# Performance work log

Hardware: AMD Instinct MI355X
Metric: run time of the kernel (lower is better)

## Reference

```python
import jax, jax.numpy as jnp
import numpy as np

B, S, D = 4, 2048, 1024
H, DK = 16, 64  # num_head, d_k = d_model // num_head
THETA = 10000.0


def apply_rope(x, positions):
    # x: [B, H, S, DK], positions: [S] int
    half = DK // 2
    inv_freq = THETA ** (-jnp.arange(half, dtype=jnp.float32) * 2.0 / DK)  # [half]
    angles = positions.astype(jnp.float32)[:, None] * inv_freq[None, :]    # [S, half]
    cos, sin = jnp.cos(angles), jnp.sin(angles)                            # [S, half]
    x1 = x[..., 0::2]  # [B,H,S,half]
    x2 = x[..., 1::2]
    r1 = x1 * cos - x2 * sin
    r2 = x1 * sin + x2 * cos
    # re-interleave pairs back to [B,H,S,DK]
    return jnp.stack([r1, r2], axis=-1).reshape(x.shape)


def setup_inputs() -> dict:
    key = jax.random.key(0)
    kx, kq, kk, kv, ko = jax.random.split(key, 5)
    scale = 1.0 / np.sqrt(D)
    return {
        "x": jax.random.normal(kx, (B, S, D), dtype=jnp.float32),
        "Wq": jax.random.normal(kq, (D, D), dtype=jnp.float32) * scale,
        "Wk": jax.random.normal(kk, (D, D), dtype=jnp.float32) * scale,
        "Wv": jax.random.normal(kv, (D, D), dtype=jnp.float32) * scale,
        "Wo": jax.random.normal(ko, (D, D), dtype=jnp.float32) * scale,
        "token_positions": jnp.arange(S, dtype=jnp.int64 if jax.config.jax_enable_x64 else jnp.int32),
    }


def reference(x, Wq, Wk, Wv, Wo, token_positions):
    # Projections (torch Linear convention: y = x @ W.T, no bias)
    def proj(x, W):
        return (x @ W.T).reshape(B, S, H, DK).transpose(0, 2, 1, 3)  # [B,H,S,DK]

    Q = apply_rope(proj(x, Wq), token_positions)
    K = apply_rope(proj(x, Wk), token_positions)
    V = proj(x, Wv)

    scores = jnp.einsum('bhqd,bhkd->bhqk', Q, K) / np.sqrt(DK)  # [B,H,S,S]
    causal = jnp.tril(jnp.ones((S, S), dtype=bool))
    scores = jnp.where(causal, scores, -jnp.inf)
    attn = jax.nn.softmax(scores, axis=-1)
    out = jnp.einsum('bhqk,bhkd->bhqd', attn, V)               # [B,H,S,DK]
    out = out.transpose(0, 2, 1, 3).reshape(B, S, D)
    return out @ Wo.T
```

## Files before the change

kernel.cpp:

```cpp
#include <hip/hip_runtime.h>
#include <math.h>

#define S_LEN  2048
#define D_DIM  1024
#define NHEAD  16
#define HDK    64
#define NBATCH 4

typedef __attribute__((ext_vector_type(8))) short bf16x8;
typedef __attribute__((ext_vector_type(4))) float f32x4;

#define MFMA16(a, b, c) __builtin_amdgcn_mfma_f32_16x16x32_bf16((a), (b), (c), 0, 0, 0)


__device__ __forceinline__ unsigned short f2bf(float f) {
    unsigned u = __float_as_uint(f);
    u += 0x7fffu + ((u >> 16) & 1u);
    return (unsigned short)(u >> 16);
}

__device__ __forceinline__ void barrier_keep_vmem() {
    asm volatile("s_waitcnt lgkmcnt(0)" ::: "memory");
    __builtin_amdgcn_s_barrier();
    __builtin_amdgcn_sched_barrier(0);
}

__global__ __launch_bounds__(256)
void convert_kernel(const float* __restrict__ src, unsigned short* __restrict__ dst, int n)
{
    int i = (blockIdx.x * 256 + threadIdx.x) * 8;
    if (i >= n) return;
    float4 f0 = *(const float4*)&src[i];
    float4 f1 = *(const float4*)&src[i + 4];
    uint4 o;
    o.x = f2bf(f0.x) | ((unsigned)f2bf(f0.y) << 16);
    o.y = f2bf(f0.z) | ((unsigned)f2bf(f0.w) << 16);
    o.z = f2bf(f1.x) | ((unsigned)f2bf(f1.y) << 16);
    o.w = f2bf(f1.z) | ((unsigned)f2bf(f1.w) << 16);
    *(uint4*)&dst[i] = o;
}

__global__ __launch_bounds__(256)
void proj_qkv_kernel(const unsigned short* __restrict__ Xb,
                     const unsigned short* __restrict__ Wqb,
                     const unsigned short* __restrict__ Wkb,
                     const unsigned short* __restrict__ Wvb,
                     const int* __restrict__ pos,
                     unsigned short* __restrict__ Qb,
                     unsigned short* __restrict__ Kb,
                     unsigned short* __restrict__ Vtb)
{
    __shared__ short As[128][40];
    __shared__ short Bs[128][40];

    const int t  = threadIdx.x;
    const int l  = t & 63;
    const int w  = t >> 6;
    const int wr = w >> 1, wc = w & 1;
    const int lm = l & 15;
    const int lk = (l >> 4) * 8;

    const int nb   = blockIdx.x;
    const int wsel = nb >> 3;
    const int n0   = (nb & 7) * 128;
    const int m0   = blockIdx.y * 128;
    const unsigned short* W = (wsel == 0) ? Wqb : (wsel == 1) ? Wkb : Wvb;

    const int sr = t >> 2;
    const int sc = (t & 3) * 8;

    f32x4 acc[4][4];
#pragma unroll
    for (int i = 0; i < 4; ++i)
#pragma unroll
        for (int j = 0; j < 4; ++j) acc[i][j] = (f32x4){0.f, 0.f, 0.f, 0.f};

    uint4 a0 = *(const uint4*)&Xb[(size_t)(m0 + sr)      * D_DIM + sc];
    uint4 a1 = *(const uint4*)&Xb[(size_t)(m0 + sr + 64) * D_DIM + sc];
    uint4 b0 = *(const uint4*)&W [(size_t)(n0 + sr)      * D_DIM + sc];
    uint4 b1 = *(const uint4*)&W [(size_t)(n0 + sr + 64) * D_DIM + sc];

    for (int k0 = 0; k0 < D_DIM; k0 += 32) {
        __syncthreads();
        *(uint4*)&As[sr][sc]      = a0;
        *(uint4*)&As[sr + 64][sc] = a1;
        *(uint4*)&Bs[sr][sc]      = b0;
        *(uint4*)&Bs[sr + 64][sc] = b1;
        if (k0 + 32 < D_DIM) {
            a0 = *(const uint4*)&Xb[(size_t)(m0 + sr)      * D_DIM + k0 + 32 + sc];
            a1 = *(const uint4*)&Xb[(size_t)(m0 + sr + 64) * D_DIM + k0 + 32 + sc];
            b0 = *(const uint4*)&W [(size_t)(n0 + sr)      * D_DIM + k0 + 32 + sc];
            b1 = *(const uint4*)&W [(size_t)(n0 + sr + 64) * D_DIM + k0 + 32 + sc];
        }
        barrier_keep_vmem();

        bf16x8 af[4], bf[4];
#pragma unroll
        for (int mt = 0; mt < 4; ++mt)
            af[mt] = *(const bf16x8*)&As[wr * 64 + mt * 16 + lm][lk];
#pragma unroll
        for (int nt = 0; nt < 4; ++nt)
            bf[nt] = *(const bf16x8*)&Bs[wc * 64 + nt * 16 + lm][lk];
#pragma unroll
        for (int mt = 0; mt < 4; ++mt)
#pragma unroll
            for (int nt = 0; nt < 4; ++nt)
                acc[mt][nt] = MFMA16(af[mt], bf[nt], acc[mt][nt]);
    }

    int dks[4], hs[4];
#pragma unroll
    for (int nt = 0; nt < 4; ++nt) {
        int col = n0 + wc * 64 + nt * 16 + lm;
        dks[nt] = col & 63;
        hs[nt]  = col >> 6;
    }

    if (wsel < 2) {
        unsigned short* Out = (wsel == 0) ? Qb : Kb;
        const float oscale = (wsel == 0) ? 0.125f : 1.0f;
        float invf[4];
#pragma unroll
        for (int nt = 0; nt < 4; ++nt)
            invf[nt] = exp2f((float)(dks[nt] >> 1) * -0.4152410119f);
#pragma unroll
        for (int mt = 0; mt < 4; ++mt)
#pragma unroll
            for (int rg = 0; rg < 4; ++rg) {
                int m = m0 + wr * 64 + mt * 16 + ((l >> 4) << 2) + rg;
                int b = m >> 11, s = m & (S_LEN - 1);
                float pf = (float)pos[s];
#pragma unroll
                for (int nt = 0; nt < 4; ++nt) {
                    float sn, cn;
                    __sincosf(pf * invf[nt], &sn, &cn);
                    float val  = acc[mt][nt][rg];
                    float part = __shfl_xor(val, 1);
                    float res  = ((dks[nt] & 1) == 0) ? val * cn - part * sn
                                                      : part * sn + val * cn;
                    Out[((size_t)(b * NHEAD + hs[nt]) * S_LEN + s) * HDK + dks[nt]] =
                        f2bf(res * oscale);
                }
            }
    } else {
#pragma unroll
        for (int mt = 0; mt < 4; ++mt)
#pragma unroll
            for (int rg = 0; rg < 4; ++rg) {
                int m = m0 + wr * 64 + mt * 16 + ((l >> 4) << 2) + rg;
                int b = m >> 11, s = m & (S_LEN - 1);
#pragma unroll
                for (int nt = 0; nt < 4; ++nt)
                    Vtb[((size_t)(b * NHEAD + hs[nt]) * HDK + dks[nt]) * S_LEN + s] =
                        f2bf(acc[mt][nt][rg]);
            }
    }
}

__global__ __launch_bounds__(512)
void attn_kernel(const unsigned short* __restrict__ Q,
                 const unsigned short* __restrict__ K,
                 const unsigned short* __restrict__ Vt,
                 unsigned short* __restrict__ AO)
{
    __shared__ short QPs[128][72];
    __shared__ short Ks[64][72];
    __shared__ short Vts[64][72];

    const int t  = threadIdx.x;
    const int l  = t & 63;
    const int w  = t >> 6;
    const int lm = l & 15;
    const int u  = l >> 4;
    const int lk = u * 8;
    const int qp = blockIdx.x, bh = blockIdx.y;

    const unsigned short* Qbh  = Q  + (size_t)bh * S_LEN * HDK;
    const unsigned short* Kbh  = K  + (size_t)bh * S_LEN * HDK;
    const unsigned short* Vtbh = Vt + (size_t)bh * S_LEN * HDK;

    const int r0 = t >> 3;
    const int ch = (t & 7) * 8;
    const int b  = bh >> 4, h = bh & 15;

    for (int ph = 0; ph < 2; ++ph) {
        const int qi    = ph ? (15 - qp) : qp;
        const int ktmax = 2 * qi + 1;

        uint4 q0 = *(const uint4*)&Qbh[(size_t)(qi * 128 + r0)      * HDK + ch];
        uint4 q1 = *(const uint4*)&Qbh[(size_t)(qi * 128 + r0 + 64) * HDK + ch];
        uint4 kreg = *(const uint4*)&Kbh [(size_t)r0 * HDK + ch];
        uint4 vreg = *(const uint4*)&Vtbh[(size_t)r0 * S_LEN + ch];

        barrier_keep_vmem();
        *(uint4*)&QPs[r0][ch]      = q0;
        *(uint4*)&QPs[r0 + 64][ch] = q1;
        barrier_keep_vmem();

        bf16x8 aq[2];
#pragma unroll
        for (int ks = 0; ks < 2; ++ks)
            aq[ks] = *(const bf16x8*)&QPs[w * 16 + lm][ks * 32 + lk];

        f32x4 o4[4];
#pragma unroll
        for (int dt = 0; dt < 4; ++dt) o4[dt] = (f32x4){0.f, 0.f, 0.f, 0.f};
        float mrow[4] = {-__builtin_inff(), -__builtin_inff(),
                         -__builtin_inff(), -__builtin_inff()};
        float lrow[4] = {0.f, 0.f, 0.f, 0.f};

        for (int kt = 0; kt <= ktmax; ++kt) {
            barrier_keep_vmem();
            *(uint4*)&Ks[r0][ch]  = kreg;
            *(uint4*)&Vts[r0][ch] = vreg;
            if (kt < ktmax) {
                kreg = *(const uint4*)&Kbh [(size_t)((kt + 1) * 64 + r0) * HDK + ch];
                vreg = *(const uint4*)&Vtbh[(size_t)r0 * S_LEN + (kt + 1) * 64 + ch];
            }
            barrier_keep_vmem();

            f32x4 sacc[4];
#pragma unroll
            for (int nt = 0; nt < 4; ++nt) sacc[nt] = (f32x4){0.f, 0.f, 0.f, 0.f};
#pragma unroll
            for (int nt = 0; nt < 4; ++nt)
#pragma unroll
                for (int ks = 0; ks < 2; ++ks) {
                    bf16x8 bk = *(const bf16x8*)&Ks[nt * 16 + lm][ks * 32 + lk];
                    sacc[nt] = MFMA16(aq[ks], bk, sacc[nt]);
                }

            const bool maskt = (kt * 64 + 63) > (qi * 128 + w * 16);
#pragma unroll
            for (int rg = 0; rg < 4; ++rg) {
                const int row_g = qi * 128 + w * 16 + u * 4 + rg;
                float sv[4];
#pragma unroll
                for (int nt = 0; nt < 4; ++nt) {
                    float x = sacc[nt][rg];
                    if (maskt && (kt * 64 + nt * 16 + lm) > row_g) x = -__builtin_inff();
                    sv[nt] = x;
                }
                float rm = fmaxf(fmaxf(sv[0], sv[1]), fmaxf(sv[2], sv[3]));
                rm = fmaxf(rm, __shfl_xor(rm, 1));
                rm = fmaxf(rm, __shfl_xor(rm, 2));
                rm = fmaxf(rm, __shfl_xor(rm, 4));
                rm = fmaxf(rm, __shfl_xor(rm, 8));
                const float mnew = fmaxf(mrow[rg], rm);
                const float corr = __expf(mrow[rg] - mnew);
                float pv[4], psum = 0.f;
#pragma unroll
                for (int nt = 0; nt < 4; ++nt) { pv[nt] = __expf(sv[nt] - mnew); psum += pv[nt]; }
                psum += __shfl_xor(psum, 1);
                psum += __shfl_xor(psum, 2);
                psum += __shfl_xor(psum, 4);
                psum += __shfl_xor(psum, 8);
                lrow[rg] = lrow[rg] * corr + psum;
                mrow[rg] = mnew;
#pragma unroll
                for (int dt = 0; dt < 4; ++dt) o4[dt][rg] *= corr;
#pragma unroll
                for (int nt = 0; nt < 4; ++nt)
                    QPs[w * 16 + u * 4 + rg][nt * 16 + lm] = (short)f2bf(pv[nt]);
            }

#pragma unroll
            for (int ks = 0; ks < 2; ++ks) {
                bf16x8 ap = *(const bf16x8*)&QPs[w * 16 + lm][ks * 32 + lk];
#pragma unroll
                for (int dt = 0; dt < 4; ++dt) {
                    bf16x8 bv = *(const bf16x8*)&Vts[dt * 16 + lm][ks * 32 + lk];
                    o4[dt] = MFMA16(ap, bv, o4[dt]);
                }
            }
        }

#pragma unroll
        for (int rg = 0; rg < 4; ++rg) {
            const int row_g = qi * 128 + w * 16 + u * 4 + rg;
            const float il = 1.0f / lrow[rg];
#pragma unroll
            for (int dt = 0; dt < 4; ++dt)
                AO[((size_t)(b * S_LEN + row_g)) * D_DIM + h * HDK + dt * 16 + lm] =
                    f2bf(o4[dt][rg] * il);
        }
    }
}

__global__ __launch_bounds__(256)
void proj_out_kernel(const unsigned short* __restrict__ Ab,
                     const unsigned short* __restrict__ Wob,
                     float* __restrict__ out)
{
    __shared__ short As[128][40];
    __shared__ short Bs[128][40];

    const int t  = threadIdx.x;
    const int l  = t & 63;
    const int w  = t >> 6;
    const int wr = w >> 1, wc = w & 1;
    const int lm = l & 15;
    const int lk = (l >> 4) * 8;
    const int n0 = blockIdx.x * 128;
    const int m0 = blockIdx.y * 128;
    const int sr = t >> 2;
    const int sc = (t & 3) * 8;

    f32x4 acc[4][4];
#pragma unroll
    for (int i = 0; i < 4; ++i)
#pragma unroll
        for (int j = 0; j < 4; ++j) acc[i][j] = (f32x4){0.f, 0.f, 0.f, 0.f};

    uint4 a0 = *(const uint4*)&Ab [(size_t)(m0 + sr)      * D_DIM + sc];
    uint4 a1 = *(const uint4*)&Ab [(size_t)(m0 + sr + 64) * D_DIM + sc];
    uint4 b0 = *(const uint4*)&Wob[(size_t)(n0 + sr)      * D_DIM + sc];
    uint4 b1 = *(const uint4*)&Wob[(size_t)(n0 + sr + 64) * D_DIM + sc];

    for (int k0 = 0; k0 < D_DIM; k0 += 32) {
        __syncthreads();
        *(uint4*)&As[sr][sc]      = a0;
        *(uint4*)&As[sr + 64][sc] = a1;
        *(uint4*)&Bs[sr][sc]      = b0;
        *(uint4*)&Bs[sr + 64][sc] = b1;
        if (k0 + 32 < D_DIM) {
            a0 = *(const uint4*)&Ab [(size_t)(m0 + sr)      * D_DIM + k0 + 32 + sc];
            a1 = *(const uint4*)&Ab [(size_t)(m0 + sr + 64) * D_DIM + k0 + 32 + sc];
            b0 = *(const uint4*)&Wob[(size_t)(n0 + sr)      * D_DIM + k0 + 32 + sc];
            b1 = *(const uint4*)&Wob[(size_t)(n0 + sr + 64) * D_DIM + k0 + 32 + sc];
        }
        barrier_keep_vmem();

        bf16x8 af[4], bf[4];
#pragma unroll
        for (int mt = 0; mt < 4; ++mt)
            af[mt] = *(const bf16x8*)&As[wr * 64 + mt * 16 + lm][lk];
#pragma unroll
        for (int nt = 0; nt < 4; ++nt)
            bf[nt] = *(const bf16x8*)&Bs[wc * 64 + nt * 16 + lm][lk];
#pragma unroll
        for (int mt = 0; mt < 4; ++mt)
#pragma unroll
            for (int nt = 0; nt < 4; ++nt)
                acc[mt][nt] = MFMA16(af[mt], bf[nt], acc[mt][nt]);
    }

#pragma unroll
    for (int mt = 0; mt < 4; ++mt)
#pragma unroll
        for (int rg = 0; rg < 4; ++rg) {
            int m = m0 + wr * 64 + mt * 16 + ((l >> 4) << 2) + rg;
#pragma unroll
            for (int nt = 0; nt < 4; ++nt)
                out[(size_t)m * D_DIM + n0 + wc * 64 + nt * 16 + lm] = acc[mt][nt][rg];
        }
}

extern "C" void kernel_launch(void* const* d_in, const int* in_sizes, int n_in,
                              void* d_out, int out_size, void* d_ws, size_t ws_size,
                              hipStream_t stream)
{
    const float* x   = (const float*)d_in[0];
    const float* Wq  = (const float*)d_in[1];
    const float* Wk  = (const float*)d_in[2];
    const float* Wv  = (const float*)d_in[3];
    const float* Wo  = (const float*)d_in[4];
    const int*   pos = (const int*)d_in[5];
    float* out = (float*)d_out;

    const size_t NX = (size_t)NBATCH * S_LEN * D_DIM;
    const size_t NW = (size_t)D_DIM * D_DIM;

    unsigned short* Xb  = (unsigned short*)d_ws;
    unsigned short* Wqb = Xb  + NX;
    unsigned short* Wkb = Wqb + NW;
    unsigned short* Wvb = Wkb + NW;
    unsigned short* Wob = Wvb + NW;
    unsigned short* Qb  = Wob + NW;
    unsigned short* Kb  = Qb  + NX;
    unsigned short* Vtb = Kb  + NX;
    unsigned short* AOb = Vtb + NX;

    dim3 blk(256);
    convert_kernel<<<dim3(4096), blk, 0, stream>>>(x,  Xb,  (int)NX);
    convert_kernel<<<dim3(512),  blk, 0, stream>>>(Wq, Wqb, (int)NW);
    convert_kernel<<<dim3(512),  blk, 0, stream>>>(Wk, Wkb, (int)NW);
    convert_kernel<<<dim3(512),  blk, 0, stream>>>(Wv, Wvb, (int)NW);
    convert_kernel<<<dim3(512),  blk, 0, stream>>>(Wo, Wob, (int)NW);

    proj_qkv_kernel<<<dim3(24, 64), blk, 0, stream>>>(Xb, Wqb, Wkb, Wvb, pos, Qb, Kb, Vtb);

    attn_kernel<<<dim3(8, NBATCH * NHEAD), dim3(512), 0, stream>>>(Qb, Kb, Vtb, AOb);

    proj_out_kernel<<<dim3(8, 64), blk, 0, stream>>>(AOb, Wob, out);
}
```

Baseline: 313.1 us.

## Merge convert launches, double GEMM K-tile, and lazily rescale softmax in attention

Combines the five fp32-to-bf16 conversion launches into one kernel indexed by block id. Both projection GEMMs now stage 64-wide K tiles with padded LDS rows, halving the number of barrier-separated iterations. The attention kernel skips the running-max correction unless some row's max grows by more than 8, which avoids exps and accumulator rescaling on most tiles. The cost is larger unnormalized probabilities, bounded by e^8, which adds some precision risk in bf16 P.

```diff
diff --git a/kernel.cpp b/kernel.cpp
--- a/kernel.cpp
+++ b/kernel.cpp
@@ -6,6 +6,8 @@
 #define NHEAD  16
 #define HDK    64
 #define NBATCH 4
+#define NXELEM (8388608)
+#define NWELEM (1048576)
 
 typedef __attribute__((ext_vector_type(8))) short bf16x8;
 typedef __attribute__((ext_vector_type(4))) float f32x4;
@@ -26,10 +28,22 @@
 }
 
 __global__ __launch_bounds__(256)
-void convert_kernel(const float* __restrict__ src, unsigned short* __restrict__ dst, int n)
+void convert_all_kernel(const float* __restrict__ x,  const float* __restrict__ wq,
+                        const float* __restrict__ wk, const float* __restrict__ wv,
+                        const float* __restrict__ wo, unsigned short* __restrict__ dstbase)
 {
-    int i = (blockIdx.x * 256 + threadIdx.x) * 8;
-    if (i >= n) return;
+    int bid = blockIdx.x;
+    const float* src;
+    unsigned short* dst;
+    int lb;
+    if (bid < 4096) { src = x; dst = dstbase; lb = bid; }
+    else {
+        int r = (bid - 4096) >> 9;
+        lb = (bid - 4096) & 511;
+        src = (r == 0) ? wq : (r == 1) ? wk : (r == 2) ? wv : wo;
+        dst = dstbase + (size_t)NXELEM + (size_t)r * NWELEM;
+    }
+    int i = (lb * 256 + threadIdx.x) * 8;
     float4 f0 = *(const float4*)&src[i];
     float4 f1 = *(const float4*)&src[i + 4];
     uint4 o;
@@ -50,8 +64,8 @@
                      unsigned short* __restrict__ Kb,
                      unsigned short* __restrict__ Vtb)
 {
-    __shared__ short As[128][40];
-    __shared__ short Bs[128][40];
+    __shared__ short As[128][72];
+    __shared__ short Bs[128][72];
 
     const int t  = threadIdx.x;
     const int l  = t & 63;
@@ -66,8 +80,8 @@
     const int m0   = blockIdx.y * 128;
     const unsigned short* W = (wsel == 0) ? Wqb : (wsel == 1) ? Wkb : Wvb;
 
-    const int sr = t >> 2;
-    const int sc = (t & 3) * 8;
+    const int sr = t >> 1;
+    const int sc = (t & 1) * 32;
 
     f32x4 acc[4][4];
 #pragma unroll
@@ -75,37 +89,43 @@
 #pragma unroll
         for (int j = 0; j < 4; ++j) acc[i][j] = (f32x4){0.f, 0.f, 0.f, 0.f};
 
-    uint4 a0 = *(const uint4*)&Xb[(size_t)(m0 + sr)      * D_DIM + sc];
-    uint4 a1 = *(const uint4*)&Xb[(size_t)(m0 + sr + 64) * D_DIM + sc];
-    uint4 b0 = *(const uint4*)&W [(size_t)(n0 + sr)      * D_DIM + sc];
-    uint4 b1 = *(const uint4*)&W [(size_t)(n0 + sr + 64) * D_DIM + sc];
-
-    for (int k0 = 0; k0 < D_DIM; k0 += 32) {
+    uint4 pa[4], pb[4];
+#pragma unroll
+    for (int j = 0; j < 4; ++j) {
+        pa[j] = *(const uint4*)&Xb[(size_t)(m0 + sr) * D_DIM + sc + j * 8];
+        pb[j] = *(const uint4*)&W [(size_t)(n0 + sr) * D_DIM + sc + j * 8];
+    }
+
+    for (int k0 = 0; k0 < D_DIM; k0 += 64) {
         __syncthreads();
-        *(uint4*)&As[sr][sc]      = a0;
-        *(uint4*)&As[sr + 64][sc] = a1;
-        *(uint4*)&Bs[sr][sc]      = b0;
-        *(uint4*)&Bs[sr + 64][sc] = b1;
-        if (k0 + 32 < D_DIM) {
-            a0 = *(const uint4*)&Xb[(size_t)(m0 + sr)      * D_DIM + k0 + 32 + sc];
-            a1 = *(const uint4*)&Xb[(size_t)(m0 + sr + 64) * D_DIM + k0 + 32 + sc];
-            b0 = *(const uint4*)&W [(size_t)(n0 + sr)      * D_DIM + k0 + 32 + sc];
-            b1 = *(const uint4*)&W [(size_t)(n0 + sr + 64) * D_DIM + k0 + 32 + sc];
+#pragma unroll
+        for (int j = 0; j < 4; ++j) {
+            *(uint4*)&As[sr][sc + j * 8] = pa[j];
+            *(uint4*)&Bs[sr][sc + j * 8] = pb[j];
+        }
+        if (k0 + 64 < D_DIM) {
+#pragma unroll
+            for (int j = 0; j < 4; ++j) {
+                pa[j] = *(const uint4*)&Xb[(size_t)(m0 + sr) * D_DIM + k0 + 64 + sc + j * 8];
+                pb[j] = *(const uint4*)&W [(size_t)(n0 + sr) * D_DIM + k0 + 64 + sc + j * 8];
+            }
         }
         barrier_keep_vmem();
 
-        bf16x8 af[4], bf[4];
-#pragma unroll
-        for (int mt = 0; mt < 4; ++mt)
-            af[mt] = *(const bf16x8*)&As[wr * 64 + mt * 16 + lm][lk];
-#pragma unroll
-        for (int nt = 0; nt < 4; ++nt)
-            bf[nt] = *(const bf16x8*)&Bs[wc * 64 + nt * 16 + lm][lk];
-#pragma unroll
-        for (int mt = 0; mt < 4; ++mt)
+#pragma unroll
+        for (int ks = 0; ks < 2; ++ks) {
+            bf16x8 bfr[4];
 #pragma unroll
             for (int nt = 0; nt < 4; ++nt)
-                acc[mt][nt] = MFMA16(af[mt], bf[nt], acc[mt][nt]);
+                bfr[nt] = *(const bf16x8*)&Bs[wc * 64 + nt * 16 + lm][ks * 32 + lk];
+#pragma unroll
+            for (int mt = 0; mt < 4; ++mt) {
+                bf16x8 afm = *(const bf16x8*)&As[wr * 64 + mt * 16 + lm][ks * 32 + lk];
+#pragma unroll
+                for (int nt = 0; nt < 4; ++nt)
+                    acc[mt][nt] = MFMA16(afm, bfr[nt], acc[mt][nt]);
+            }
+        }
     }
 
     int dks[4], hs[4];
@@ -231,37 +251,53 @@
                 }
 
             const bool maskt = (kt * 64 + 63) > (qi * 128 + w * 16);
+            float rm4[4];
 #pragma unroll
             for (int rg = 0; rg < 4; ++rg) {
-                const int row_g = qi * 128 + w * 16 + u * 4 + rg;
-                float sv[4];
-#pragma unroll
-                for (int nt = 0; nt < 4; ++nt) {
-                    float x = sacc[nt][rg];
-                    if (maskt && (kt * 64 + nt * 16 + lm) > row_g) x = -__builtin_inff();
-                    sv[nt] = x;
-                }
-                float rm = fmaxf(fmaxf(sv[0], sv[1]), fmaxf(sv[2], sv[3]));
+                if (maskt) {
+                    const int row_g = qi * 128 + w * 16 + u * 4 + rg;
+#pragma unroll
+                    for (int nt = 0; nt < 4; ++nt)
+                        if ((kt * 64 + nt * 16 + lm) > row_g)
+                            sacc[nt][rg] = -__builtin_inff();
+                }
+                float rm = fmaxf(fmaxf(sacc[0][rg], sacc[1][rg]),
+                                 fmaxf(sacc[2][rg], sacc[3][rg]));
                 rm = fmaxf(rm, __shfl_xor(rm, 1));
                 rm = fmaxf(rm, __shfl_xor(rm, 2));
                 rm = fmaxf(rm, __shfl_xor(rm, 4));
                 rm = fmaxf(rm, __shfl_xor(rm, 8));
-                const float mnew = fmaxf(mrow[rg], rm);
-                const float corr = __expf(mrow[rg] - mnew);
-                float pv[4], psum = 0.f;
-#pragma unroll
-                for (int nt = 0; nt < 4; ++nt) { pv[nt] = __expf(sv[nt] - mnew); psum += pv[nt]; }
+                rm4[rg] = rm;
+            }
+            int need = 0;
+#pragma unroll
+            for (int rg = 0; rg < 4; ++rg)
+                need |= (rm4[rg] > mrow[rg] + 8.0f) ? 1 : 0;
+            if (__any(need)) {
+#pragma unroll
+                for (int rg = 0; rg < 4; ++rg) {
+                    const float mnew = fmaxf(mrow[rg], rm4[rg]);
+                    const float corr = __expf(mrow[rg] - mnew);
+                    lrow[rg] *= corr;
+                    mrow[rg] = mnew;
+#pragma unroll
+                    for (int dt = 0; dt < 4; ++dt) o4[dt][rg] *= corr;
+                }
+            }
+#pragma unroll
+            for (int rg = 0; rg < 4; ++rg) {
+                float psum = 0.f;
+#pragma unroll
+                for (int nt = 0; nt < 4; ++nt) {
+                    float p = __expf(sacc[nt][rg] - mrow[rg]);
+                    psum += p;
+                    QPs[w * 16 + u * 4 + rg][nt * 16 + lm] = (short)f2bf(p);
+                }
                 psum += __shfl_xor(psum, 1);
                 psum += __shfl_xor(psum, 2);
                 psum += __shfl_xor(psum, 4);
                 psum += __shfl_xor(psum, 8);
-                lrow[rg] = lrow[rg] * corr + psum;
-                mrow[rg] = mnew;
-#pragma unroll
-                for (int dt = 0; dt < 4; ++dt) o4[dt][rg] *= corr;
-#pragma unroll
-                for (int nt = 0; nt < 4; ++nt)
-                    QPs[w * 16 + u * 4 + rg][nt * 16 + lm] = (short)f2bf(pv[nt]);
+                lrow[rg] += psum;
             }
 
 #pragma unroll
@@ -292,8 +328,8 @@
                      const unsigned short* __restrict__ Wob,
                      float* __restrict__ out)
 {
-    __shared__ short As[128][40];
-    __shared__ short Bs[128][40];
+    __shared__ short As[128][72];
+    __shared__ short Bs[128][72];
 
     const int t  = threadIdx.x;
     const int l  = t & 63;
@@ -303,8 +339,8 @@
     const int lk = (l >> 4) * 8;
     const int n0 = blockIdx.x * 128;
     const int m0 = blockIdx.y * 128;
-    const int sr = t >> 2;
-    const int sc = (t & 3) * 8;
+    const int sr = t >> 1;
+    const int sc = (t & 1) * 32;
 
     f32x4 acc[4][4];
 #pragma unroll
@@ -312,37 +348,43 @@
 #pragma unroll
         for (int j = 0; j < 4; ++j) acc[i][j] = (f32x4){0.f, 0.f, 0.f, 0.f};
 
-    uint4 a0 = *(const uint4*)&Ab [(size_t)(m0 + sr)      * D_DIM + sc];
-    uint4 a1 = *(const uint4*)&Ab [(size_t)(m0 + sr + 64) * D_DIM + sc];
-    uint4 b0 = *(const uint4*)&Wob[(size_t)(n0 + sr)      * D_DIM + sc];
-    uint4 b1 = *(const uint4*)&Wob[(size_t)(n0 + sr + 64) * D_DIM + sc];
-
-    for (int k0 = 0; k0 < D_DIM; k0 += 32) {
+    uint4 pa[4], pb[4];
+#pragma unroll
+    for (int j = 0; j < 4; ++j) {
+        pa[j] = *(const uint4*)&Ab [(size_t)(m0 + sr) * D_DIM + sc + j * 8];
+        pb[j] = *(const uint4*)&Wob[(size_t)(n0 + sr) * D_DIM + sc + j * 8];
+    }
+
+    for (int k0 = 0; k0 < D_DIM; k0 += 64) {
         __syncthreads();
-        *(uint4*)&As[sr][sc]      = a0;
-        *(uint4*)&As[sr + 64][sc] = a1;
-        *(uint4*)&Bs[sr][sc]      = b0;
-        *(uint4*)&Bs[sr + 64][sc] = b1;
-        if (k0 + 32 < D_DIM) {
-            a0 = *(const uint4*)&Ab [(size_t)(m0 + sr)      * D_DIM + k0 + 32 + sc];
-            a1 = *(const uint4*)&Ab [(size_t)(m0 + sr + 64) * D_DIM + k0 + 32 + sc];
-            b0 = *(const uint4*)&Wob[(size_t)(n0 + sr)      * D_DIM + k0 + 32 + sc];
-            b1 = *(const uint4*)&Wob[(size_t)(n0 + sr + 64) * D_DIM + k0 + 32 + sc];
+#pragma unroll
+        for (int j = 0; j < 4; ++j) {
+            *(uint4*)&As[sr][sc + j * 8] = pa[j];
+            *(uint4*)&Bs[sr][sc + j * 8] = pb[j];
+        }
+        if (k0 + 64 < D_DIM) {
+#pragma unroll
+            for (int j = 0; j < 4; ++j) {
+                pa[j] = *(const uint4*)&Ab [(size_t)(m0 + sr) * D_DIM + k0 + 64 + sc + j * 8];
+                pb[j] = *(const uint4*)&Wob[(size_t)(n0 + sr) * D_DIM + k0 + 64 + sc + j * 8];
+            }
         }
         barrier_keep_vmem();
 
-        bf16x8 af[4], bf[4];
-#pragma unroll
-        for (int mt = 0; mt < 4; ++mt)
-            af[mt] = *(const bf16x8*)&As[wr * 64 + mt * 16 + lm][lk];
-#pragma unroll
-        for (int nt = 0; nt < 4; ++nt)
-            bf[nt] = *(const bf16x8*)&Bs[wc * 64 + nt * 16 + lm][lk];
-#pragma unroll
-        for (int mt = 0; mt < 4; ++mt)
+#pragma unroll
+        for (int ks = 0; ks < 2; ++ks) {
+            bf16x8 bfr[4];
 #pragma unroll
             for (int nt = 0; nt < 4; ++nt)
-                acc[mt][nt] = MFMA16(af[mt], bf[nt], acc[mt][nt]);
+                bfr[nt] = *(const bf16x8*)&Bs[wc * 64 + nt * 16 + lm][ks * 32 + lk];
+#pragma unroll
+            for (int mt = 0; mt < 4; ++mt) {
+                bf16x8 afm = *(const bf16x8*)&As[wr * 64 + mt * 16 + lm][ks * 32 + lk];
+#pragma unroll
+                for (int nt = 0; nt < 4; ++nt)
+                    acc[mt][nt] = MFMA16(afm, bfr[nt], acc[mt][nt]);
+            }
+        }
     }
 
 #pragma unroll
@@ -368,8 +410,7 @@
     const int*   pos = (const int*)d_in[5];
     float* out = (float*)d_out;
 
-    const size_t NX = (size_t)NBATCH * S_LEN * D_DIM;
-    const size_t NW = (size_t)D_DIM * D_DIM;
+    const size_t NX = NXELEM, NW = NWELEM;
 
     unsigned short* Xb  = (unsigned short*)d_ws;
     unsigned short* Wqb = Xb  + NX;
@@ -381,16 +422,11 @@
     unsigned short* Vtb = Kb  + NX;
     unsigned short* AOb = Vtb + NX;
 
-    dim3 blk(256);
-    convert_kernel<<<dim3(4096), blk, 0, stream>>>(x,  Xb,  (int)NX);
-    convert_kernel<<<dim3(512),  blk, 0, stream>>>(Wq, Wqb, (int)NW);
-    convert_kernel<<<dim3(512),  blk, 0, stream>>>(Wk, Wkb, (int)NW);
-    convert_kernel<<<dim3(512),  blk, 0, stream>>>(Wv, Wvb, (int)NW);
-    convert_kernel<<<dim3(512),  blk, 0, stream>>>(Wo, Wob, (int)NW);
-
-    proj_qkv_kernel<<<dim3(24, 64), blk, 0, stream>>>(Xb, Wqb, Wkb, Wvb, pos, Qb, Kb, Vtb);
+    convert_all_kernel<<<dim3(6144), dim3(256), 0, stream>>>(x, Wq, Wk, Wv, Wo, Xb);
+
+    proj_qkv_kernel<<<dim3(24, 64), dim3(256), 0, stream>>>(Xb, Wqb, Wkb, Wvb, pos, Qb, Kb, Vtb);
 
     attn_kernel<<<dim3(8, NBATCH * NHEAD), dim3(512), 0, stream>>>(Qb, Kb, Vtb, AOb);
 
-    proj_out_kernel<<<dim3(8, 64), blk, 0, stream>>>(AOb, Wob, out);
-}
+    proj_out_kernel<<<dim3(8, 64), dim3(256), 0, stream>>>(AOb, Wob, out);
+}
```

New measurement: 515.6 us. 1.65x slower.
